# Optimization experiments

Measured on AMD Instinct MI355X. Metric: run time of the kernel, lower is better.

## Reference

```python
import jax, jax.numpy as jnp
import numpy as np

LN_EPS = 1e-6

def hsigmoid(v):
    # HSigmoid with bias=3, divisor=6: clamp((v+3)/6, 0, 1)
    return jnp.clip((v + 3.0) / 6.0, 0.0, 1.0)

def setup_inputs() -> dict:
    key = jax.random.key(0)
    ks = jax.random.split(key, 10)
    b, c, h, w = 8, 512, 64, 64
    s = lambda fan: 1.0 / np.sqrt(fan)
    return {
        "x": jax.random.normal(ks[0], (b, c, h, w), jnp.float32),
        "w_b1": jax.random.normal(ks[1], (c // 2, c), jnp.float32) * s(c),
        "b_b1": jax.random.normal(ks[2], (c // 2,), jnp.float32) * 0.01,
        "w_b2": jax.random.normal(ks[3], (c, c // 2), jnp.float32) * s(c // 2),
        "b_b2": jax.random.normal(ks[4], (c,), jnp.float32) * 0.01,
        "w_conv1": jax.random.normal(ks[5], (1, c), jnp.float32) * s(c),
        "ln_g": jnp.ones((c,), jnp.float32),
        "ln_b": jnp.zeros((c,), jnp.float32),
        "sk_w1": jax.random.normal(ks[6], (c // 2, c), jnp.float32) * s(c),
        "sk_w2": jax.random.normal(ks[7], (c, c // 2), jnp.float32) * s(c // 2),
        "res_w": jax.random.normal(ks[8], (c, c), jnp.float32) * s(c),
    }

def reference(x, w_b1, b_b1, w_b2, b_b2, w_conv1, ln_g, ln_b, sk_w1, sk_w2, res_w):
    b, c, h, w = x.shape
    # --- channel attention: GAP -> 1x1 conv+ReLU -> 1x1 conv+HSigmoid -> LN over c ---
    g = x.mean(axis=(2, 3))                                  # (b, c)
    ca = jax.nn.relu(g @ w_b1.T + b_b1)                      # (b, c/2)
    ca = hsigmoid(ca @ w_b2.T + b_b2)                        # (b, c)
    mu = ca.mean(axis=-1, keepdims=True)
    var = ca.var(axis=-1, keepdims=True)
    ca = (ca - mu) / jnp.sqrt(var + LN_EPS) * ln_g + ln_b    # LayerNorm over channels
    channel_attn = ca[:, :, None, None]                      # (b, c, 1, 1)
    # --- spatial attention: 1x1 conv (c->1, no bias) + HSigmoid ---
    spatial_attn = hsigmoid(jnp.einsum('bchw,c->bhw', x, w_conv1[0]))[:, None]  # (b,1,h,w)
    # --- parallel attention: torch float // 2 == floor((a+b)/2) ---
    par_attn = jnp.floor((spatial_attn + channel_attn) / 2.0)  # (b, c, h, w)
    # --- sequence attention: bmm outer product (b,c,1)x(b,1,hw) ---
    seq_attn = channel_attn * spatial_attn                     # (b, c, h, w)
    # --- SK module: GAP(sum) -> conv+ReLU -> conv+ReLU -> softmax over c ---
    u = (seq_attn + par_attn).mean(axis=(2, 3))                # (b, c)
    u = jax.nn.relu(u @ sk_w1.T)
    u = jax.nn.relu(u @ sk_w2.T)
    a = jax.nn.softmax(u, axis=1)[:, :, None, None]            # (b, c, 1, 1)
    selected_attn = seq_attn * a + par_attn * (1.0 - a)        # (b, c, h, w)
    # --- self attention: spatial sum + 1x1 residual conv ---
    self_attn = selected_attn.sum(axis=(2, 3))[:, :, None, None] \
        + jnp.einsum('bchw,oc->bohw', x, res_w)                # (b, c, h, w)
    return x * selected_attn + self_attn
```

## Files before the change

### kernel.cpp

```cpp
#include <hip/hip_runtime.h>
#include <stdint.h>

#define HW 4096
#define NC 512
#define NB 8

typedef __attribute__((ext_vector_type(8))) short short8;
typedef __attribute__((ext_vector_type(4))) float f32x4;

__device__ __forceinline__ unsigned short f2bf(float f) {
  unsigned int u = __builtin_bit_cast(unsigned int, f);
  unsigned int r = (u + 0x7FFFu + ((u >> 16) & 1u)) >> 16;
  return (unsigned short)r;
}
__device__ __forceinline__ float hsig(float v) {
  return fminf(fmaxf((v + 3.0f) * (1.0f / 6.0f), 0.0f), 1.0f);
}

__device__ __forceinline__ void gload16(const void* g, void* l) {
  __builtin_amdgcn_global_load_lds(
      (const __attribute__((address_space(1))) unsigned int*)g,
      (__attribute__((address_space(3))) unsigned int*)l, 16, 0, 0);
}

__device__ __forceinline__ float block_reduce_sum(float v, volatile float* red) {
  int t = threadIdx.x;
#pragma unroll
  for (int m = 1; m < 64; m <<= 1) v += __shfl_xor(v, m);
  if ((t & 63) == 0) red[t >> 6] = v;
  __syncthreads();
  v = red[0] + red[1] + red[2] + red[3];
  __syncthreads();
  return v;
}
__device__ __forceinline__ float block_reduce_max(float v, volatile float* red) {
  int t = threadIdx.x;
#pragma unroll
  for (int m = 1; m < 64; m <<= 1) v = fmaxf(v, __shfl_xor(v, m));
  if ((t & 63) == 0) red[t >> 6] = v;
  __syncthreads();
  v = fmaxf(fmaxf(red[0], red[1]), fmaxf(red[2], red[3]));
  __syncthreads();
  return v;
}

__device__ __forceinline__ float dot_chunks(const float4* __restrict__ wr,
                                            const float4* __restrict__ vl,
                                            int nchunks) {
  float p0 = 0.f, p1 = 0.f, p2 = 0.f, p3 = 0.f;
#pragma unroll 8
  for (int i = 0; i < nchunks; i += 4) {
    float4 w0 = wr[i], w1 = wr[i + 1], w2 = wr[i + 2], w3 = wr[i + 3];
    float4 a0 = vl[i], a1 = vl[i + 1], a2 = vl[i + 2], a3 = vl[i + 3];
    p0 += w0.x * a0.x + w0.y * a0.y + w0.z * a0.z + w0.w * a0.w;
    p1 += w1.x * a1.x + w1.y * a1.y + w1.z * a1.z + w1.w * a1.w;
    p2 += w2.x * a2.x + w2.y * a2.y + w2.z * a2.z + w2.w * a2.w;
    p3 += w3.x * a3.x + w3.y * a3.y + w3.z * a3.z + w3.w * a3.w;
  }
  return (p0 + p1) + (p2 + p3);
}

__global__ __launch_bounds__(256) void k1_stats_transpose(
    const float* __restrict__ x, const float* __restrict__ w_conv1,
    const float* __restrict__ res_w,
    float* __restrict__ g_sum, float* __restrict__ spat,
    unsigned short* __restrict__ xTS, unsigned short* __restrict__ wbfS) {
  __shared__ float sp_lds[16][64];
  __shared__ unsigned short t_lds[64 * 72];
  const int t = threadIdx.x;
  const int b = blockIdx.z;
  const int c0 = blockIdx.y * 64;
  const int h0 = blockIdx.x * 64;
  const int cg = t >> 4;
  const int hg = t & 15;

  float vv[4][4];
  float wc[4];
  const float* xb = x + ((size_t)(b * NC + c0 + cg * 4) * HW) + h0 + hg * 4;
#pragma unroll
  for (int i = 0; i < 4; i++) {
    float4 v = *(const float4*)(xb + (size_t)i * HW);
    vv[i][0] = v.x; vv[i][1] = v.y; vv[i][2] = v.z; vv[i][3] = v.w;
    wc[i] = w_conv1[c0 + cg * 4 + i];
  }
#pragma unroll
  for (int i = 0; i < 4; i++) {
    float s = vv[i][0] + vv[i][1] + vv[i][2] + vv[i][3];
    s += __shfl_xor(s, 1); s += __shfl_xor(s, 2);
    s += __shfl_xor(s, 4); s += __shfl_xor(s, 8);
    if (hg == 0) atomicAdd(&g_sum[b * NC + c0 + cg * 4 + i], s);
  }
  {
    float4 sp;
    sp.x = vv[0][0] * wc[0] + vv[1][0] * wc[1] + vv[2][0] * wc[2] + vv[3][0] * wc[3];
    sp.y = vv[0][1] * wc[0] + vv[1][1] * wc[1] + vv[2][1] * wc[2] + vv[3][1] * wc[3];
    sp.z = vv[0][2] * wc[0] + vv[1][2] * wc[1] + vv[2][2] * wc[2] + vv[3][2] * wc[3];
    sp.w = vv[0][3] * wc[0] + vv[1][3] * wc[1] + vv[2][3] * wc[2] + vv[3][3] * wc[3];
    *(float4*)&sp_lds[cg][hg * 4] = sp;
  }
#pragma unroll
  for (int j = 0; j < 4; j++) {
    ushort4 u;
    u.x = f2bf(vv[0][j]); u.y = f2bf(vv[1][j]);
    u.z = f2bf(vv[2][j]); u.w = f2bf(vv[3][j]);
    *(ushort4*)&t_lds[(hg * 4 + j) * 72 + cg * 4] = u;
  }
  __syncthreads();
  if (t < 64) {
    float s = 0.f;
#pragma unroll
    for (int i = 0; i < 16; i++) s += sp_lds[i][t];
    atomicAdd(&spat[b * HW + h0 + t], s);
  }
  const int w = t >> 6, l = t & 63;
#pragma unroll
  for (int ff = w; ff < 8; ff += 4) {
    const int fr = ff >> 1, fk = ff & 1;
    short8 v = *(const short8*)&t_lds[(fr * 16 + (l & 15)) * 72 + (fk * 4 + (l >> 4)) * 8];
    size_t tile = (size_t)(b * 256 + (h0 >> 4) + fr) * 16 + (c0 >> 5) + fk;
    *(short8*)(xTS + tile * 512 + l * 8) = v;
  }
  if (b == 0 && t < 64) {
    const int q = blockIdx.y * 64 + blockIdx.x;
    float4 a = *(const float4*)(res_w + (size_t)q * 512 + t * 8);
    float4 c2 = *(const float4*)(res_w + (size_t)q * 512 + t * 8 + 4);
    short8 v;
    v[0] = (short)f2bf(a.x); v[1] = (short)f2bf(a.y);
    v[2] = (short)f2bf(a.z); v[3] = (short)f2bf(a.w);
    v[4] = (short)f2bf(c2.x); v[5] = (short)f2bf(c2.y);
    v[6] = (short)f2bf(c2.z); v[7] = (short)f2bf(c2.w);
    const int lq = (q & 15) + ((t & 3) << 4);
    *(short8*)(wbfS + ((size_t)(q >> 4) * 16 + (t >> 2)) * 512 + lq * 8) = v;
  }
}

__global__ __launch_bounds__(256) void k2a_mv1(
    const float* __restrict__ g_sum, const float* __restrict__ spat,
    const float* __restrict__ w_b1, const float* __restrict__ b_b1,
    float* __restrict__ s_out, float* __restrict__ Ssum, float* __restrict__ ca1) {
  __shared__ float g_l[512];
  const int t = threadIdx.x;
  const int b = blockIdx.x >> 2, q = blockIdx.x & 3;
  {
    int idx = b * HW + q * 1024 + t * 4;
    float4 v = *(const float4*)(spat + idx);
    float4 o;
    o.x = hsig(v.x); o.y = hsig(v.y); o.z = hsig(v.z); o.w = hsig(v.w);
    *(float4*)(s_out + idx) = o;
    float sum = o.x + o.y + o.z + o.w;
#pragma unroll
    for (int m = 1; m < 64; m <<= 1) sum += __shfl_xor(sum, m);
    if ((t & 63) == 0) atomicAdd(&Ssum[b], sum);
  }
  g_l[t] = g_sum[b * NC + t] * (1.0f / 4096.0f);
  g_l[t + 256] = g_sum[b * NC + t + 256] * (1.0f / 4096.0f);
  __syncthreads();
  const int o = q * 64 + (t >> 2), kq = t & 3;
  float sum = dot_chunks((const float4*)(w_b1 + (size_t)o * 512 + kq * 128),
                         (const float4*)(g_l + kq * 128), 32);
  sum += __shfl_xor(sum, 1);
  sum += __shfl_xor(sum, 2);
  if (kq == 0) ca1[b * 256 + o] = fmaxf(sum + b_b1[o], 0.0f);
}

__global__ __launch_bounds__(256) void k2_mv2_ln(
    const float* __restrict__ ca1, const float* __restrict__ w_b2,
    const float* __restrict__ b_b2, const float* __restrict__ ln_g,
    const float* __restrict__ ln_b, float* __restrict__ t_out) {
  __shared__ float ca1_l[256];
  __shared__ float red[4];
  const int b = blockIdx.x, t = threadIdx.x;
  ca1_l[t] = ca1[b * 256 + t];
  __syncthreads();
  float ca[2];
#pragma unroll
  for (int h = 0; h < 2; h++) {
    int o = t + h * 256;
    float acc = dot_chunks((const float4*)(w_b2 + (size_t)o * 256),
                           (const float4*)ca1_l, 64);
    ca[h] = hsig(acc + b_b2[o]);
  }
  float S = block_reduce_sum(ca[0] + ca[1], red);
  float SQ = block_reduce_sum(ca[0] * ca[0] + ca[1] * ca[1], red);
  float mu = S * (1.0f / 512.0f);
  float var = SQ * (1.0f / 512.0f) - mu * mu;
  float rstd = rsqrtf(var + 1e-6f);
#pragma unroll
  for (int h = 0; h < 2; h++) {
    int o = t + h * 256;
    t_out[b * NC + o] = (ca[h] - mu) * rstd * ln_g[o] + ln_b[o];
  }
}

__global__ __launch_bounds__(256) void k2b_floorsum(
    const float* __restrict__ s, const float* __restrict__ t_arr, float* __restrict__ P) {
  __shared__ float s_l[4096];
  const int t = threadIdx.x;
  const int b = blockIdx.y;
  const int c0 = blockIdx.x * 16;
  const float* sb = s + b * HW;
#pragma unroll
  for (int i = 0; i < 16; i++) s_l[t + i * 256] = sb[t + i * 256];
  __syncthreads();
  const int w = t >> 6, l = t & 63;
#pragma unroll
  for (int j = 0; j < 4; j++) {
    int c = c0 + w * 4 + j;
    float tc = t_arr[b * NC + c];
    float sum = 0.f;
#pragma unroll 8
    for (int i = 0; i < 64; i++) sum += floorf((s_l[l + i * 64] + tc) * 0.5f);
#pragma unroll
    for (int m = 1; m < 64; m <<= 1) sum += __shfl_xor(sum, m);
    if (l == 0) P[b * NC + c] = sum;
  }
}

__global__ __launch_bounds__(256) void k2c1_mv(
    const float* __restrict__ t_arr, const float* __restrict__ P,
    const float* __restrict__ Ssum, const float* __restrict__ sk_w1,
    float* __restrict__ u1) {
  __shared__ float u_l[512];
  const int t = threadIdx.x;
  const int b = blockIdx.x >> 2, q = blockIdx.x & 3;
  const float Ss = Ssum[b];
#pragma unroll
  for (int h = 0; h < 2; h++) {
    int c = t + h * 256;
    u_l[c] = (t_arr[b * NC + c] * Ss + P[b * NC + c]) * (1.0f / 4096.0f);
  }
  __syncthreads();
  const int o = q * 64 + (t >> 2), kq = t & 3;
  float sum = dot_chunks((const float4*)(sk_w1 + (size_t)o * 512 + kq * 128),
                         (const float4*)(u_l + kq * 128), 32);
  sum += __shfl_xor(sum, 1);
  sum += __shfl_xor(sum, 2);
  if (kq == 0) u1[b * 256 + o] = fmaxf(sum, 0.0f);
}

__global__ __launch_bounds__(256) void k2c2_select(
    const float* __restrict__ u1, const float* __restrict__ sk_w2,
    const float* __restrict__ t_arr, const float* __restrict__ P,
    const float* __restrict__ Ssum, float* __restrict__ coef) {
  __shared__ float u1_l[256];
  __shared__ float red[4];
  const int b = blockIdx.x, t = threadIdx.x;
  const float Ss = Ssum[b];
  u1_l[t] = u1[b * 256 + t];
  __syncthreads();
  float u2[2];
#pragma unroll
  for (int h = 0; h < 2; h++) {
    int o = t + h * 256;
    float acc = dot_chunks((const float4*)(sk_w2 + (size_t)o * 256),
                           (const float4*)u1_l, 64);
    u2[h] = fmaxf(acc, 0.0f);
  }
  float M = block_reduce_max(fmaxf(u2[0], u2[1]), red);
  float e0 = __expf(u2[0] - M), e1 = __expf(u2[1] - M);
  float Z = block_reduce_sum(e0 + e1, red);
  float inv = 1.0f / Z;
#pragma unroll
  for (int h = 0; h < 2; h++) {
    int o = t + h * 256;
    float a = (h == 0 ? e0 : e1) * inv;
    float tc = t_arr[b * NC + o];
    float Pv = P[b * NC + o];
    float c1 = a * tc;
    float c2 = 1.0f - a;
    float c3 = c1 * Ss + c2 * Pv;
    float4 cf = {c1, c2, c3, tc};
    *(float4*)(coef + (size_t)(b * NC + o) * 4) = cf;
  }
}

__global__ __launch_bounds__(256, 4) void k3_gemm_epilogue(
    const unsigned short* __restrict__ wbfS, const unsigned short* __restrict__ xTS,
    const float* __restrict__ x, const float* __restrict__ s,
    const float* __restrict__ coef, float* __restrict__ out) {
  __shared__ __align__(16) char smem[32768];
  const int t = threadIdx.x;
  const int bx = blockIdx.x, mz = blockIdx.y, b = blockIdx.z;
  const int w = t >> 6, l = t & 63;
  const int wm = w >> 1, wn = w & 1;
  const int l16 = l & 15, quad = l >> 4;

  f32x4 acc[4][4];
#pragma unroll
  for (int mi = 0; mi < 4; mi++)
#pragma unroll
    for (int ni = 0; ni < 4; ni++) {
      f32x4 z = {0.f, 0.f, 0.f, 0.f};
      acc[mi][ni] = z;
    }

  const char* gA0 = (const char*)wbfS + ((size_t)(mz * 8 + 2 * w) * 16) * 1024 + l * 16;
  const char* gA1 = gA0 + 16 * 1024;
  const char* gB0 = (const char*)xTS + ((size_t)(b * 256 + bx * 8 + 2 * w) * 16) * 1024 + l * 16;
  const char* gB1 = gB0 + 16 * 1024;
  char* lA0 = smem + (2 * w) * 1024;
  char* lA1 = smem + (2 * w + 1) * 1024;
  char* lB0 = smem + 8192 + (2 * w) * 1024;
  char* lB1 = smem + 8192 + (2 * w + 1) * 1024;
  const char* pA = smem + wm * 4096 + l * 16;
  const char* pB = smem + 8192 + wn * 4096 + l * 16;

#define K3_STAGE(buf, kk) do {                                  \
    gload16(gA0 + (kk) * 1024, lA0 + (buf) * 16384);            \
    gload16(gA1 + (kk) * 1024, lA1 + (buf) * 16384);            \
    gload16(gB0 + (kk) * 1024, lB0 + (buf) * 16384);            \
    gload16(gB1 + (kk) * 1024, lB1 + (buf) * 16384);            \
  } while (0)

#define K3_COMPUTE(buf) do {                                    \
    short8 af[4], bfr[4];                                       \
    _Pragma("unroll")                                           \
    for (int mi = 0; mi < 4; mi++)                              \
      af[mi] = *(const short8*)(pA + (buf) * 16384 + mi * 1024);\
    _Pragma("unroll")                                           \
    for (int ni = 0; ni < 4; ni++)                              \
      bfr[ni] = *(const short8*)(pB + (buf) * 16384 + ni * 1024);\
    _Pragma("unroll")                                           \
    for (int mi = 0; mi < 4; mi++)                              \
      _Pragma("unroll")                                         \
      for (int ni = 0; ni < 4; ni++)                            \
        acc[mi][ni] = __builtin_amdgcn_mfma_f32_16x16x32_bf16(  \
            af[mi], bfr[ni], acc[mi][ni], 0, 0, 0);             \
  } while (0)

  K3_STAGE(0, 0);
  __syncthreads();
#pragma unroll
  for (int kk = 0; kk < 16; kk += 2) {
    K3_STAGE(1, kk + 1);
    K3_COMPUTE(0);
    __syncthreads();
    if (kk + 2 < 16) K3_STAGE(0, kk + 2);
    K3_COMPUTE(1);
    __syncthreads();
  }

  float* eb = (float*)smem + w * 1088;
  const int row = l >> 2, cb = (l & 3) * 16;
  const int colb = bx * 128 + wn * 64 + cb;
  const float* sp = s + b * HW + colb;
  float4 sv[4];
#pragma unroll
  for (int j = 0; j < 4; j++) sv[j] = *(const float4*)(sp + 4 * j);
#pragma unroll
  for (int mi = 0; mi < 4; mi++) {
#pragma unroll
    for (int ni = 0; ni < 4; ni++)
#pragma unroll
      for (int r = 0; r < 4; r++)
        eb[(quad * 4 + r) * 68 + ni * 16 + l16] = acc[mi][ni][r];
    const int o = mz * 128 + wm * 64 + mi * 16 + row;
    float4 cf = *(const float4*)(coef + (size_t)(b * NC + o) * 4);
    const size_t rbase = (size_t)(b * NC + o) * HW + colb;
#pragma unroll
    for (int j = 0; j < 4; j++) {
      f32x4 y = *(f32x4*)&eb[row * 68 + cb + 4 * j];
      float4 svj = sv[j];
      float4 xv = *(const float4*)(x + rbase + 4 * j);
      float4 ov;
      ov.x = xv.x * (cf.x * svj.x + cf.y * floorf((svj.x + cf.w) * 0.5f)) + cf.z + y.x;
      ov.y = xv.y * (cf.x * svj.y + cf.y * floorf((svj.y + cf.w) * 0.5f)) + cf.z + y.y;
      ov.z = xv.z * (cf.x * svj.z + cf.y * floorf((svj.z + cf.w) * 0.5f)) + cf.z + y.z;
      ov.w = xv.w * (cf.x * svj.w + cf.y * floorf((svj.w + cf.w) * 0.5f)) + cf.z + y.w;
      *(float4*)(out + rbase + 4 * j) = ov;
    }
  }
#undef K3_STAGE
#undef K3_COMPUTE
}

extern "C" void kernel_launch(void* const* d_in, const int* in_sizes, int n_in,
                              void* d_out, int out_size, void* d_ws, size_t ws_size,
                              hipStream_t stream) {
  const float* x       = (const float*)d_in[0];
  const float* w_b1    = (const float*)d_in[1];
  const float* b_b1    = (const float*)d_in[2];
  const float* w_b2    = (const float*)d_in[3];
  const float* b_b2    = (const float*)d_in[4];
  const float* w_conv1 = (const float*)d_in[5];
  const float* ln_g    = (const float*)d_in[6];
  const float* ln_b    = (const float*)d_in[7];
  const float* sk_w1   = (const float*)d_in[8];
  const float* sk_w2   = (const float*)d_in[9];
  const float* res_w   = (const float*)d_in[10];
  float* out = (float*)d_out;
  char* ws = (char*)d_ws;

  float* g_sum = (float*)(ws + 0x00000);
  float* spat  = (float*)(ws + 0x08000);
  float* Ssum  = (float*)(ws + 0x28000);
  float* t_arr = (float*)(ws + 0x29000);
  float* P     = (float*)(ws + 0x30000);
  float* coef  = (float*)(ws + 0x38000);
  float* s     = (float*)(ws + 0x50000);
  float* ca1   = (float*)(ws + 0x70000);
  float* u1    = (float*)(ws + 0x72000);
  unsigned short* wbfS = (unsigned short*)(ws + 0x80000);
  unsigned short* xTS  = (unsigned short*)(ws + 0x100000);

  hipMemsetAsync(ws, 0, 0x28040, stream);
  k1_stats_transpose<<<dim3(64, 8, 8), 256, 0, stream>>>(x, w_conv1, res_w, g_sum, spat, xTS, wbfS);
  k2a_mv1<<<32, 256, 0, stream>>>(g_sum, spat, w_b1, b_b1, s, Ssum, ca1);
  k2_mv2_ln<<<8, 256, 0, stream>>>(ca1, w_b2, b_b2, ln_g, ln_b, t_arr);
  k2b_floorsum<<<dim3(32, 8), 256, 0, stream>>>(s, t_arr, P);
  k2c1_mv<<<32, 256, 0, stream>>>(t_arr, P, Ssum, sk_w1, u1);
  k2c2_select<<<8, 256, 0, stream>>>(u1, sk_w2, t_arr, P, Ssum, coef);
  k3_gemm_epilogue<<<dim3(32, 4, 8), 256, 0, stream>>>(wbfS, xTS, x, s, coef, out);
}
```

Baseline: 238.4 us.

## Fuse small attention kernels and triple-buffer the GEMM K-loop

Merges the four small per-batch matvec/LayerNorm/softmax kernels into two 512-thread kernels, which removes two launches and the intermediate ca1/u1 round trips through global memory. The Ssum atomics become a single block reduction. The bf16 MFMA GEMM moves from a double-buffered loop with two barriers per step to a three-stage LDS ring that waits with an explicit vmcnt and uses one barrier per K step. In exchange the GEMM needs 48KB of LDS and its occupancy hint drops from 4 to 3, while the fused small kernels run only 8 blocks each.

```diff
diff --git a/kernel.cpp b/kernel.cpp
--- a/kernel.cpp
+++ b/kernel.cpp
@@ -23,23 +23,27 @@
       (__attribute__((address_space(3))) unsigned int*)l, 16, 0, 0);
 }
 
-__device__ __forceinline__ float block_reduce_sum(float v, volatile float* red) {
+__device__ __forceinline__ float block_reduce_sum8(float v, volatile float* red) {
   int t = threadIdx.x;
 #pragma unroll
   for (int m = 1; m < 64; m <<= 1) v += __shfl_xor(v, m);
   if ((t & 63) == 0) red[t >> 6] = v;
   __syncthreads();
-  v = red[0] + red[1] + red[2] + red[3];
+  v = 0.f;
+#pragma unroll
+  for (int i = 0; i < 8; i++) v += red[i];
   __syncthreads();
   return v;
 }
-__device__ __forceinline__ float block_reduce_max(float v, volatile float* red) {
+__device__ __forceinline__ float block_reduce_max8(float v, volatile float* red) {
   int t = threadIdx.x;
 #pragma unroll
   for (int m = 1; m < 64; m <<= 1) v = fmaxf(v, __shfl_xor(v, m));
   if ((t & 63) == 0) red[t >> 6] = v;
   __syncthreads();
-  v = fmaxf(fmaxf(red[0], red[1]), fmaxf(red[2], red[3]));
+  v = red[0];
+#pragma unroll
+  for (int i = 1; i < 8; i++) v = fmaxf(v, red[i]);
   __syncthreads();
   return v;
 }
@@ -134,62 +138,46 @@
   }
 }
 
-__global__ __launch_bounds__(256) void k2a_mv1(
+__global__ __launch_bounds__(512) void k2f1(
     const float* __restrict__ g_sum, const float* __restrict__ spat,
     const float* __restrict__ w_b1, const float* __restrict__ b_b1,
-    float* __restrict__ s_out, float* __restrict__ Ssum, float* __restrict__ ca1) {
-  __shared__ float g_l[512];
-  const int t = threadIdx.x;
-  const int b = blockIdx.x >> 2, q = blockIdx.x & 3;
-  {
-    int idx = b * HW + q * 1024 + t * 4;
-    float4 v = *(const float4*)(spat + idx);
+    const float* __restrict__ w_b2, const float* __restrict__ b_b2,
+    const float* __restrict__ ln_g, const float* __restrict__ ln_b,
+    float* __restrict__ s_out, float* __restrict__ Ssum,
+    float* __restrict__ t_out) {
+  __shared__ float vec_l[512];
+  __shared__ float ca1_l[256];
+  __shared__ float red[8];
+  const int b = blockIdx.x, t = threadIdx.x;
+  float part = 0.f;
+#pragma unroll
+  for (int i = 0; i < 2; i++) {
+    int idx = i * 2048 + t * 4;
+    float4 v = *(const float4*)(spat + b * HW + idx);
     float4 o;
     o.x = hsig(v.x); o.y = hsig(v.y); o.z = hsig(v.z); o.w = hsig(v.w);
-    *(float4*)(s_out + idx) = o;
-    float sum = o.x + o.y + o.z + o.w;
-#pragma unroll
-    for (int m = 1; m < 64; m <<= 1) sum += __shfl_xor(sum, m);
-    if ((t & 63) == 0) atomicAdd(&Ssum[b], sum);
-  }
-  g_l[t] = g_sum[b * NC + t] * (1.0f / 4096.0f);
-  g_l[t + 256] = g_sum[b * NC + t + 256] * (1.0f / 4096.0f);
-  __syncthreads();
-  const int o = q * 64 + (t >> 2), kq = t & 3;
-  float sum = dot_chunks((const float4*)(w_b1 + (size_t)o * 512 + kq * 128),
-                         (const float4*)(g_l + kq * 128), 32);
-  sum += __shfl_xor(sum, 1);
-  sum += __shfl_xor(sum, 2);
-  if (kq == 0) ca1[b * 256 + o] = fmaxf(sum + b_b1[o], 0.0f);
-}
-
-__global__ __launch_bounds__(256) void k2_mv2_ln(
-    const float* __restrict__ ca1, const float* __restrict__ w_b2,
-    const float* __restrict__ b_b2, const float* __restrict__ ln_g,
-    const float* __restrict__ ln_b, float* __restrict__ t_out) {
-  __shared__ float ca1_l[256];
-  __shared__ float red[4];
-  const int b = blockIdx.x, t = threadIdx.x;
-  ca1_l[t] = ca1[b * 256 + t];
-  __syncthreads();
-  float ca[2];
-#pragma unroll
-  for (int h = 0; h < 2; h++) {
-    int o = t + h * 256;
-    float acc = dot_chunks((const float4*)(w_b2 + (size_t)o * 256),
-                           (const float4*)ca1_l, 64);
-    ca[h] = hsig(acc + b_b2[o]);
-  }
-  float S = block_reduce_sum(ca[0] + ca[1], red);
-  float SQ = block_reduce_sum(ca[0] * ca[0] + ca[1] * ca[1], red);
+    *(float4*)(s_out + b * HW + idx) = o;
+    part += o.x + o.y + o.z + o.w;
+  }
+  vec_l[t] = g_sum[b * NC + t] * (1.0f / 4096.0f);
+  float Ss = block_reduce_sum8(part, red);
+  if (t == 0) Ssum[b] = Ss;
+  {
+    const int o = t >> 1, half = t & 1;
+    float acc = dot_chunks((const float4*)(w_b1 + (size_t)o * 512 + half * 256),
+                           (const float4*)(vec_l + half * 256), 64);
+    acc += __shfl_xor(acc, 1);
+    if (half == 0) ca1_l[o] = fmaxf(acc + b_b1[o], 0.0f);
+  }
+  __syncthreads();
+  float ca = hsig(dot_chunks((const float4*)(w_b2 + (size_t)t * 256),
+                             (const float4*)ca1_l, 64) + b_b2[t]);
+  float S = block_reduce_sum8(ca, red);
+  float SQ = block_reduce_sum8(ca * ca, red);
   float mu = S * (1.0f / 512.0f);
   float var = SQ * (1.0f / 512.0f) - mu * mu;
   float rstd = rsqrtf(var + 1e-6f);
-#pragma unroll
-  for (int h = 0; h < 2; h++) {
-    int o = t + h * 256;
-    t_out[b * NC + o] = (ca[h] - mu) * rstd * ln_g[o] + ln_b[o];
-  }
+  t_out[b * NC + t] = (ca - mu) * rstd * ln_g[t] + ln_b[t];
 }
 
 __global__ __launch_bounds__(256) void k2b_floorsum(
@@ -216,69 +204,45 @@
   }
 }
 
-__global__ __launch_bounds__(256) void k2c1_mv(
+__global__ __launch_bounds__(512) void k2f2(
     const float* __restrict__ t_arr, const float* __restrict__ P,
     const float* __restrict__ Ssum, const float* __restrict__ sk_w1,
-    float* __restrict__ u1) {
+    const float* __restrict__ sk_w2, float* __restrict__ coef) {
   __shared__ float u_l[512];
-  const int t = threadIdx.x;
-  const int b = blockIdx.x >> 2, q = blockIdx.x & 3;
-  const float Ss = Ssum[b];
-#pragma unroll
-  for (int h = 0; h < 2; h++) {
-    int c = t + h * 256;
-    u_l[c] = (t_arr[b * NC + c] * Ss + P[b * NC + c]) * (1.0f / 4096.0f);
-  }
-  __syncthreads();
-  const int o = q * 64 + (t >> 2), kq = t & 3;
-  float sum = dot_chunks((const float4*)(sk_w1 + (size_t)o * 512 + kq * 128),
-                         (const float4*)(u_l + kq * 128), 32);
-  sum += __shfl_xor(sum, 1);
-  sum += __shfl_xor(sum, 2);
-  if (kq == 0) u1[b * 256 + o] = fmaxf(sum, 0.0f);
-}
-
-__global__ __launch_bounds__(256) void k2c2_select(
-    const float* __restrict__ u1, const float* __restrict__ sk_w2,
-    const float* __restrict__ t_arr, const float* __restrict__ P,
-    const float* __restrict__ Ssum, float* __restrict__ coef) {
   __shared__ float u1_l[256];
-  __shared__ float red[4];
+  __shared__ float red[8];
   const int b = blockIdx.x, t = threadIdx.x;
   const float Ss = Ssum[b];
-  u1_l[t] = u1[b * 256 + t];
-  __syncthreads();
-  float u2[2];
-#pragma unroll
-  for (int h = 0; h < 2; h++) {
-    int o = t + h * 256;
-    float acc = dot_chunks((const float4*)(sk_w2 + (size_t)o * 256),
-                           (const float4*)u1_l, 64);
-    u2[h] = fmaxf(acc, 0.0f);
-  }
-  float M = block_reduce_max(fmaxf(u2[0], u2[1]), red);
-  float e0 = __expf(u2[0] - M), e1 = __expf(u2[1] - M);
-  float Z = block_reduce_sum(e0 + e1, red);
-  float inv = 1.0f / Z;
-#pragma unroll
-  for (int h = 0; h < 2; h++) {
-    int o = t + h * 256;
-    float a = (h == 0 ? e0 : e1) * inv;
-    float tc = t_arr[b * NC + o];
-    float Pv = P[b * NC + o];
-    float c1 = a * tc;
-    float c2 = 1.0f - a;
-    float c3 = c1 * Ss + c2 * Pv;
-    float4 cf = {c1, c2, c3, tc};
-    *(float4*)(coef + (size_t)(b * NC + o) * 4) = cf;
-  }
-}
-
-__global__ __launch_bounds__(256, 4) void k3_gemm_epilogue(
+  const float tc = t_arr[b * NC + t];
+  const float Pv = P[b * NC + t];
+  u_l[t] = (tc * Ss + Pv) * (1.0f / 4096.0f);
+  __syncthreads();
+  {
+    const int o = t >> 1, half = t & 1;
+    float acc = dot_chunks((const float4*)(sk_w1 + (size_t)o * 512 + half * 256),
+                           (const float4*)(u_l + half * 256), 64);
+    acc += __shfl_xor(acc, 1);
+    if (half == 0) u1_l[o] = fmaxf(acc, 0.0f);
+  }
+  __syncthreads();
+  float u2 = fmaxf(dot_chunks((const float4*)(sk_w2 + (size_t)t * 256),
+                              (const float4*)u1_l, 64), 0.0f);
+  float M = block_reduce_max8(u2, red);
+  float e = __expf(u2 - M);
+  float Z = block_reduce_sum8(e, red);
+  float a = e / Z;
+  float c1 = a * tc;
+  float c2 = 1.0f - a;
+  float c3 = c1 * Ss + c2 * Pv;
+  float4 cf = {c1, c2, c3, tc};
+  *(float4*)(coef + (size_t)(b * NC + t) * 4) = cf;
+}
+
+__global__ __launch_bounds__(256, 3) void k3_gemm_epilogue(
     const unsigned short* __restrict__ wbfS, const unsigned short* __restrict__ xTS,
     const float* __restrict__ x, const float* __restrict__ s,
     const float* __restrict__ coef, float* __restrict__ out) {
-  __shared__ __align__(16) char smem[32768];
+  __shared__ __align__(16) char smem[49152];
   const int t = threadIdx.x;
   const int bx = blockIdx.x, mz = blockIdx.y, b = blockIdx.z;
   const int w = t >> 6, l = t & 63;
@@ -298,28 +262,24 @@
   const char* gA1 = gA0 + 16 * 1024;
   const char* gB0 = (const char*)xTS + ((size_t)(b * 256 + bx * 8 + 2 * w) * 16) * 1024 + l * 16;
   const char* gB1 = gB0 + 16 * 1024;
-  char* lA0 = smem + (2 * w) * 1024;
-  char* lA1 = smem + (2 * w + 1) * 1024;
-  char* lB0 = smem + 8192 + (2 * w) * 1024;
-  char* lB1 = smem + 8192 + (2 * w + 1) * 1024;
-  const char* pA = smem + wm * 4096 + l * 16;
-  const char* pB = smem + 8192 + wn * 4096 + l * 16;
-
-#define K3_STAGE(buf, kk) do {                                  \
-    gload16(gA0 + (kk) * 1024, lA0 + (buf) * 16384);            \
-    gload16(gA1 + (kk) * 1024, lA1 + (buf) * 16384);            \
-    gload16(gB0 + (kk) * 1024, lB0 + (buf) * 16384);            \
-    gload16(gB1 + (kk) * 1024, lB1 + (buf) * 16384);            \
+
+#define K3_STAGE(base, kk) do {                                 \
+    gload16(gA0 + (kk) * 1024, (base) + (2 * w) * 1024);        \
+    gload16(gA1 + (kk) * 1024, (base) + (2 * w + 1) * 1024);    \
+    gload16(gB0 + (kk) * 1024, (base) + 8192 + (2 * w) * 1024); \
+    gload16(gB1 + (kk) * 1024, (base) + 8192 + (2 * w + 1) * 1024); \
   } while (0)
 
-#define K3_COMPUTE(buf) do {                                    \
+#define K3_COMPUTE(base) do {                                   \
+    const char* pA = (base) + wm * 4096 + l * 16;               \
+    const char* pB = (base) + 8192 + wn * 4096 + l * 16;        \
     short8 af[4], bfr[4];                                       \
     _Pragma("unroll")                                           \
     for (int mi = 0; mi < 4; mi++)                              \
-      af[mi] = *(const short8*)(pA + (buf) * 16384 + mi * 1024);\
+      af[mi] = *(const short8*)(pA + mi * 1024);                \
     _Pragma("unroll")                                           \
     for (int ni = 0; ni < 4; ni++)                              \
-      bfr[ni] = *(const short8*)(pB + (buf) * 16384 + ni * 1024);\
+      bfr[ni] = *(const short8*)(pB + ni * 1024);               \
     _Pragma("unroll")                                           \
     for (int mi = 0; mi < 4; mi++)                              \
       _Pragma("unroll")                                         \
@@ -328,17 +288,23 @@
             af[mi], bfr[ni], acc[mi][ni], 0, 0, 0);             \
   } while (0)
 
-  K3_STAGE(0, 0);
-  __syncthreads();
-#pragma unroll
-  for (int kk = 0; kk < 16; kk += 2) {
-    K3_STAGE(1, kk + 1);
-    K3_COMPUTE(0);
-    __syncthreads();
-    if (kk + 2 < 16) K3_STAGE(0, kk + 2);
-    K3_COMPUTE(1);
-    __syncthreads();
-  }
+  K3_STAGE(smem, 0);
+  K3_STAGE(smem + 16384, 1);
+#pragma unroll
+  for (int kk = 0; kk < 16; kk++) {
+    const int cur = kk % 3;
+    const int nxt = (kk + 2) % 3;
+    if (kk < 15) {
+      asm volatile("s_waitcnt vmcnt(4)" ::: "memory");
+    } else {
+      asm volatile("s_waitcnt vmcnt(0)" ::: "memory");
+    }
+    __builtin_amdgcn_s_barrier();
+    __builtin_amdgcn_sched_barrier(0);
+    if (kk < 14) K3_STAGE(smem + nxt * 16384, kk + 2);
+    K3_COMPUTE(smem + cur * 16384);
+  }
+  __syncthreads();
 
   float* eb = (float*)smem + w * 1088;
   const int row = l >> 2, cb = (l & 3) * 16;
@@ -398,17 +364,13 @@
   float* P     = (float*)(ws + 0x30000);
   float* coef  = (float*)(ws + 0x38000);
   float* s     = (float*)(ws + 0x50000);
-  float* ca1   = (float*)(ws + 0x70000);
-  float* u1    = (float*)(ws + 0x72000);
   unsigned short* wbfS = (unsigned short*)(ws + 0x80000);
   unsigned short* xTS  = (unsigned short*)(ws + 0x100000);
 
-  hipMemsetAsync(ws, 0, 0x28040, stream);
+  hipMemsetAsync(ws, 0, 0x28000, stream);
   k1_stats_transpose<<<dim3(64, 8, 8), 256, 0, stream>>>(x, w_conv1, res_w, g_sum, spat, xTS, wbfS);
-  k2a_mv1<<<32, 256, 0, stream>>>(g_sum, spat, w_b1, b_b1, s, Ssum, ca1);
-  k2_mv2_ln<<<8, 256, 0, stream>>>(ca1, w_b2, b_b2, ln_g, ln_b, t_arr);
+  k2f1<<<8, 512, 0, stream>>>(g_sum, spat, w_b1, b_b1, w_b2, b_b2, ln_g, ln_b, s, Ssum, t_arr);
   k2b_floorsum<<<dim3(32, 8), 256, 0, stream>>>(s, t_arr, P);
-  k2c1_mv<<<32, 256, 0, stream>>>(t_arr, P, Ssum, sk_w1, u1);
-  k2c2_select<<<8, 256, 0, stream>>>(u1, sk_w2, t_arr, P, Ssum, coef);
+  k2f2<<<8, 512, 0, stream>>>(t_arr, P, Ssum, sk_w1, sk_w2, coef);
   k3_gemm_epilogue<<<dim3(32, 4, 8), 256, 0, stream>>>(wbfS, xTS, x, s, coef, out);
 }
```

Result: slower. 259.9 us (+9.0%).

## Spread small matvecs across many blocks with one wave per output

Applied to the files above, without the earlier changes.

The four small matrix-vector stages (channel-attention MLP and SK MLP) are rewritten so that each 64-lane wave computes one output row with a full-wave shuffle reduction, launched over 512 or 1024 blocks instead of 8 or 32. The layer-norm and softmax steps are split into their own tiny kernels, reading intermediates from new workspace buffers. The aim is to use the whole GPU for these latency-bound stages instead of a handful of CUs. The cost is two extra kernel launches and extra global round-trips for the intermediates.

```diff
diff --git a/kernel.cpp b/kernel.cpp
--- a/kernel.cpp
+++ b/kernel.cpp
@@ -23,6 +23,12 @@
       (__attribute__((address_space(3))) unsigned int*)l, 16, 0, 0);
 }
 
+__device__ __forceinline__ float wave_reduce(float p) {
+#pragma unroll
+  for (int m = 1; m < 64; m <<= 1) p += __shfl_xor(p, m);
+  return p;
+}
+
 __device__ __forceinline__ float block_reduce_sum(float v, volatile float* red) {
   int t = threadIdx.x;
 #pragma unroll
@@ -42,22 +48,6 @@
   v = fmaxf(fmaxf(red[0], red[1]), fmaxf(red[2], red[3]));
   __syncthreads();
   return v;
-}
-
-__device__ __forceinline__ float dot_chunks(const float4* __restrict__ wr,
-                                            const float4* __restrict__ vl,
-                                            int nchunks) {
-  float p0 = 0.f, p1 = 0.f, p2 = 0.f, p3 = 0.f;
-#pragma unroll 8
-  for (int i = 0; i < nchunks; i += 4) {
-    float4 w0 = wr[i], w1 = wr[i + 1], w2 = wr[i + 2], w3 = wr[i + 3];
-    float4 a0 = vl[i], a1 = vl[i + 1], a2 = vl[i + 2], a3 = vl[i + 3];
-    p0 += w0.x * a0.x + w0.y * a0.y + w0.z * a0.z + w0.w * a0.w;
-    p1 += w1.x * a1.x + w1.y * a1.y + w1.z * a1.z + w1.w * a1.w;
-    p2 += w2.x * a2.x + w2.y * a2.y + w2.z * a2.z + w2.w * a2.w;
-    p3 += w3.x * a3.x + w3.y * a3.y + w3.z * a3.z + w3.w * a3.w;
-  }
-  return (p0 + p1) + (p2 + p3);
 }
 
 __global__ __launch_bounds__(256) void k1_stats_transpose(
@@ -134,62 +124,63 @@
   }
 }
 
-__global__ __launch_bounds__(256) void k2a_mv1(
+
+__global__ __launch_bounds__(256) void k2_mv1(
     const float* __restrict__ g_sum, const float* __restrict__ spat,
     const float* __restrict__ w_b1, const float* __restrict__ b_b1,
-    float* __restrict__ s_out, float* __restrict__ Ssum, float* __restrict__ ca1) {
-  __shared__ float g_l[512];
-  const int t = threadIdx.x;
-  const int b = blockIdx.x >> 2, q = blockIdx.x & 3;
-  {
-    int idx = b * HW + q * 1024 + t * 4;
-    float4 v = *(const float4*)(spat + idx);
-    float4 o;
-    o.x = hsig(v.x); o.y = hsig(v.y); o.z = hsig(v.z); o.w = hsig(v.w);
-    *(float4*)(s_out + idx) = o;
-    float sum = o.x + o.y + o.z + o.w;
-#pragma unroll
-    for (int m = 1; m < 64; m <<= 1) sum += __shfl_xor(sum, m);
-    if ((t & 63) == 0) atomicAdd(&Ssum[b], sum);
-  }
-  g_l[t] = g_sum[b * NC + t] * (1.0f / 4096.0f);
-  g_l[t + 256] = g_sum[b * NC + t + 256] * (1.0f / 4096.0f);
-  __syncthreads();
-  const int o = q * 64 + (t >> 2), kq = t & 3;
-  float sum = dot_chunks((const float4*)(w_b1 + (size_t)o * 512 + kq * 128),
-                         (const float4*)(g_l + kq * 128), 32);
-  sum += __shfl_xor(sum, 1);
-  sum += __shfl_xor(sum, 2);
-  if (kq == 0) ca1[b * 256 + o] = fmaxf(sum + b_b1[o], 0.0f);
-}
-
-__global__ __launch_bounds__(256) void k2_mv2_ln(
+    float* __restrict__ s_out, float* __restrict__ Ssum,
+    float* __restrict__ ca1) {
+  const int l = threadIdx.x & 63;
+  const int W = blockIdx.x * 4 + (threadIdx.x >> 6);
+  const int b = W >> 8, o = W & 255;
+  const float* wr = w_b1 + (size_t)o * 512 + l * 8;
+  float4 wa = *(const float4*)wr;
+  float4 wb = *(const float4*)(wr + 4);
+  const float* gr = g_sum + b * NC + l * 8;
+  float4 ga = *(const float4*)gr;
+  float4 gb = *(const float4*)(gr + 4);
+  float p = wa.x * ga.x + wa.y * ga.y + wa.z * ga.z + wa.w * ga.w +
+            wb.x * gb.x + wb.y * gb.y + wb.z * gb.z + wb.w * gb.w;
+  p = wave_reduce(p);
+  if (l == 0) ca1[b * 256 + o] = fmaxf(p * (1.0f / 4096.0f) + b_b1[o], 0.0f);
+  if (blockIdx.x < 32) {
+    const int b2 = blockIdx.x >> 2;
+    const int i4 = (blockIdx.x & 3) * 256 + threadIdx.x;
+    float4 v = ((const float4*)(spat + (size_t)b2 * HW))[i4];
+    float4 os;
+    os.x = hsig(v.x); os.y = hsig(v.y); os.z = hsig(v.z); os.w = hsig(v.w);
+    ((float4*)(s_out + (size_t)b2 * HW))[i4] = os;
+    float sum = wave_reduce(os.x + os.y + os.z + os.w);
+    if (l == 0) atomicAdd(&Ssum[b2], sum);
+  }
+}
+
+__global__ __launch_bounds__(256) void k2_mv2(
     const float* __restrict__ ca1, const float* __restrict__ w_b2,
-    const float* __restrict__ b_b2, const float* __restrict__ ln_g,
+    const float* __restrict__ b_b2, float* __restrict__ ca2) {
+  const int l = threadIdx.x & 63;
+  const int W = blockIdx.x * 4 + (threadIdx.x >> 6);
+  const int b = W >> 9, o = W & 511;
+  float4 wv = ((const float4*)(w_b2 + (size_t)o * 256))[l];
+  float4 cv = ((const float4*)(ca1 + b * 256))[l];
+  float p = wv.x * cv.x + wv.y * cv.y + wv.z * cv.z + wv.w * cv.w;
+  p = wave_reduce(p);
+  if (l == 0) ca2[b * NC + o] = hsig(p + b_b2[o]);
+}
+
+__global__ __launch_bounds__(256) void k2_ln(
+    const float* __restrict__ ca2, const float* __restrict__ ln_g,
     const float* __restrict__ ln_b, float* __restrict__ t_out) {
-  __shared__ float ca1_l[256];
   __shared__ float red[4];
   const int b = blockIdx.x, t = threadIdx.x;
-  ca1_l[t] = ca1[b * 256 + t];
-  __syncthreads();
-  float ca[2];
-#pragma unroll
-  for (int h = 0; h < 2; h++) {
-    int o = t + h * 256;
-    float acc = dot_chunks((const float4*)(w_b2 + (size_t)o * 256),
-                           (const float4*)ca1_l, 64);
-    ca[h] = hsig(acc + b_b2[o]);
-  }
-  float S = block_reduce_sum(ca[0] + ca[1], red);
-  float SQ = block_reduce_sum(ca[0] * ca[0] + ca[1] * ca[1], red);
+  float v0 = ca2[b * NC + t], v1 = ca2[b * NC + t + 256];
+  float S = block_reduce_sum(v0 + v1, red);
+  float SQ = block_reduce_sum(v0 * v0 + v1 * v1, red);
   float mu = S * (1.0f / 512.0f);
   float var = SQ * (1.0f / 512.0f) - mu * mu;
   float rstd = rsqrtf(var + 1e-6f);
-#pragma unroll
-  for (int h = 0; h < 2; h++) {
-    int o = t + h * 256;
-    t_out[b * NC + o] = (ca[h] - mu) * rstd * ln_g[o] + ln_b[o];
-  }
+  t_out[b * NC + t] = (v0 - mu) * rstd * ln_g[t] + ln_b[t];
+  t_out[b * NC + t + 256] = (v1 - mu) * rstd * ln_g[t + 256] + ln_b[t + 256];
 }
 
 __global__ __launch_bounds__(256) void k2b_floorsum(
@@ -216,48 +207,55 @@
   }
 }
 
-__global__ __launch_bounds__(256) void k2c1_mv(
+__global__ __launch_bounds__(256) void k2_sk1(
     const float* __restrict__ t_arr, const float* __restrict__ P,
     const float* __restrict__ Ssum, const float* __restrict__ sk_w1,
     float* __restrict__ u1) {
-  __shared__ float u_l[512];
-  const int t = threadIdx.x;
-  const int b = blockIdx.x >> 2, q = blockIdx.x & 3;
+  const int l = threadIdx.x & 63;
+  const int W = blockIdx.x * 4 + (threadIdx.x >> 6);
+  const int b = W >> 8, o = W & 255;
   const float Ss = Ssum[b];
-#pragma unroll
-  for (int h = 0; h < 2; h++) {
-    int c = t + h * 256;
-    u_l[c] = (t_arr[b * NC + c] * Ss + P[b * NC + c]) * (1.0f / 4096.0f);
-  }
-  __syncthreads();
-  const int o = q * 64 + (t >> 2), kq = t & 3;
-  float sum = dot_chunks((const float4*)(sk_w1 + (size_t)o * 512 + kq * 128),
-                         (const float4*)(u_l + kq * 128), 32);
-  sum += __shfl_xor(sum, 1);
-  sum += __shfl_xor(sum, 2);
-  if (kq == 0) u1[b * 256 + o] = fmaxf(sum, 0.0f);
-}
-
-__global__ __launch_bounds__(256) void k2c2_select(
+  const float* wr = sk_w1 + (size_t)o * 512 + l * 8;
+  float4 wa = *(const float4*)wr;
+  float4 wb = *(const float4*)(wr + 4);
+  const float* tr = t_arr + b * NC + l * 8;
+  const float* pr = P + b * NC + l * 8;
+  float4 ta = *(const float4*)tr, tb = *(const float4*)(tr + 4);
+  float4 Pa = *(const float4*)pr, Pb = *(const float4*)(pr + 4);
+  float4 ua, ub;
+  ua.x = ta.x * Ss + Pa.x; ua.y = ta.y * Ss + Pa.y;
+  ua.z = ta.z * Ss + Pa.z; ua.w = ta.w * Ss + Pa.w;
+  ub.x = tb.x * Ss + Pb.x; ub.y = tb.y * Ss + Pb.y;
+  ub.z = tb.z * Ss + Pb.z; ub.w = tb.w * Ss + Pb.w;
+  float p = wa.x * ua.x + wa.y * ua.y + wa.z * ua.z + wa.w * ua.w +
+            wb.x * ub.x + wb.y * ub.y + wb.z * ub.z + wb.w * ub.w;
+  p = wave_reduce(p) * (1.0f / 4096.0f);
+  if (l == 0) u1[b * 256 + o] = fmaxf(p, 0.0f);
+}
+
+__global__ __launch_bounds__(256) void k2_sk2(
     const float* __restrict__ u1, const float* __restrict__ sk_w2,
-    const float* __restrict__ t_arr, const float* __restrict__ P,
-    const float* __restrict__ Ssum, float* __restrict__ coef) {
-  __shared__ float u1_l[256];
+    float* __restrict__ u2) {
+  const int l = threadIdx.x & 63;
+  const int W = blockIdx.x * 4 + (threadIdx.x >> 6);
+  const int b = W >> 9, o = W & 511;
+  float4 wv = ((const float4*)(sk_w2 + (size_t)o * 256))[l];
+  float4 cv = ((const float4*)(u1 + b * 256))[l];
+  float p = wv.x * cv.x + wv.y * cv.y + wv.z * cv.z + wv.w * cv.w;
+  p = wave_reduce(p);
+  if (l == 0) u2[b * NC + o] = fmaxf(p, 0.0f);
+}
+
+__global__ __launch_bounds__(256) void k2_smx(
+    const float* __restrict__ u2, const float* __restrict__ t_arr,
+    const float* __restrict__ P, const float* __restrict__ Ssum,
+    float* __restrict__ coef) {
   __shared__ float red[4];
   const int b = blockIdx.x, t = threadIdx.x;
   const float Ss = Ssum[b];
-  u1_l[t] = u1[b * 256 + t];
-  __syncthreads();
-  float u2[2];
-#pragma unroll
-  for (int h = 0; h < 2; h++) {
-    int o = t + h * 256;
-    float acc = dot_chunks((const float4*)(sk_w2 + (size_t)o * 256),
-                           (const float4*)u1_l, 64);
-    u2[h] = fmaxf(acc, 0.0f);
-  }
-  float M = block_reduce_max(fmaxf(u2[0], u2[1]), red);
-  float e0 = __expf(u2[0] - M), e1 = __expf(u2[1] - M);
+  float v0 = u2[b * NC + t], v1 = u2[b * NC + t + 256];
+  float M = block_reduce_max(fmaxf(v0, v1), red);
+  float e0 = __expf(v0 - M), e1 = __expf(v1 - M);
   float Z = block_reduce_sum(e0 + e1, red);
   float inv = 1.0f / Z;
 #pragma unroll
@@ -400,15 +398,19 @@
   float* s     = (float*)(ws + 0x50000);
   float* ca1   = (float*)(ws + 0x70000);
   float* u1    = (float*)(ws + 0x72000);
+  float* ca2   = (float*)(ws + 0x74000);
+  float* u2    = (float*)(ws + 0x78000);
   unsigned short* wbfS = (unsigned short*)(ws + 0x80000);
   unsigned short* xTS  = (unsigned short*)(ws + 0x100000);
 
   hipMemsetAsync(ws, 0, 0x28040, stream);
   k1_stats_transpose<<<dim3(64, 8, 8), 256, 0, stream>>>(x, w_conv1, res_w, g_sum, spat, xTS, wbfS);
-  k2a_mv1<<<32, 256, 0, stream>>>(g_sum, spat, w_b1, b_b1, s, Ssum, ca1);
-  k2_mv2_ln<<<8, 256, 0, stream>>>(ca1, w_b2, b_b2, ln_g, ln_b, t_arr);
+  k2_mv1<<<512, 256, 0, stream>>>(g_sum, spat, w_b1, b_b1, s, Ssum, ca1);
+  k2_mv2<<<1024, 256, 0, stream>>>(ca1, w_b2, b_b2, ca2);
+  k2_ln<<<8, 256, 0, stream>>>(ca2, ln_g, ln_b, t_arr);
   k2b_floorsum<<<dim3(32, 8), 256, 0, stream>>>(s, t_arr, P);
-  k2c1_mv<<<32, 256, 0, stream>>>(t_arr, P, Ssum, sk_w1, u1);
-  k2c2_select<<<8, 256, 0, stream>>>(u1, sk_w2, t_arr, P, Ssum, coef);
+  k2_sk1<<<512, 256, 0, stream>>>(t_arr, P, Ssum, sk_w1, u1);
+  k2_sk2<<<1024, 256, 0, stream>>>(u1, sk_w2, u2);
+  k2_smx<<<8, 256, 0, stream>>>(u2, t_arr, P, Ssum, coef);
   k3_gemm_epilogue<<<dim3(32, 4, 8), 256, 0, stream>>>(wbfS, xTS, x, s, coef, out);
 }
```

New measurement: 196.0 us. -17.8%, faster.
